# Optimization experiments

Hardware: AMD Instinct MI355X
Metric: run time of the kernel (lower is better)

Reference implementation:

```python
import jax, jax.numpy as jnp
import numpy as np

DEPTH = 16
HID = 256
INP = 256
K = 2  # arity of the complete binary tree
TOTAL = (1 << (DEPTH + 1)) - 1  # 131071 nodes, level-order indexed


def setup_inputs() -> dict:
    key = jax.random.key(0)
    ks = jax.random.split(key, 14)
    s = 1.0 / np.sqrt(HID)
    inp = {
        "x": jax.random.normal(ks[0], (TOTAL, INP), jnp.float32),
        "Wi": jax.random.normal(ks[1], (HID, INP), jnp.float32) * s,
        "bi": jax.random.normal(ks[2], (HID,), jnp.float32) * s,
        "Wf": jax.random.normal(ks[3], (HID, INP), jnp.float32) * s,
        "bf": jax.random.normal(ks[4], (HID,), jnp.float32) * s,
        "Wo": jax.random.normal(ks[5], (HID, INP), jnp.float32) * s,
        "bo": jax.random.normal(ks[6], (HID,), jnp.float32) * s,
        "Wu": jax.random.normal(ks[7], (HID, INP), jnp.float32) * s,
        "bu": jax.random.normal(ks[8], (HID,), jnp.float32) * s,
        "Ui": jax.random.normal(ks[9], (HID, HID), jnp.float32) * s,
        "Uo": jax.random.normal(ks[10], (HID, HID), jnp.float32) * s,
        "Uu": jax.random.normal(ks[11], (HID, HID), jnp.float32) * s,
        "Wfk": jax.random.normal(ks[12], (K, HID, HID), jnp.float32) * s,
        "depth": DEPTH,
    }
    return inp


def reference(x, Wi, bi, Wf, bf, Wo, bo, Wu, bu, Ui, Uo, Uu, Wfk, depth):
    sig = jax.nn.sigmoid
    H = Ui.shape[0]
    # leaf level: leaf_forward (no recurrent terms)
    start, n = (1 << depth) - 1, 1 << depth
    xs = x[start:start + n]                      # [n, INP]
    i = sig(xs @ Wi.T + bi)
    o = sig(xs @ Wo.T + bo)
    u = jnp.tanh(xs @ Wu.T + bu)
    c = i * u
    h = o * jnp.tanh(c)
    # internal levels, bottom-up
    for d in range(depth - 1, -1, -1):
        start, n = (1 << d) - 1, 1 << d
        xs = x[start:start + n]                  # [n, INP]
        hc = h.reshape(n, K, H)                  # children h (level-order)
        cc = c.reshape(n, K, H)                  # children c
        Hs = hc.sum(axis=1)                      # sum over children, [n, H]
        i = sig(xs @ Wi.T + bi + Hs @ Ui.T)
        o = sig(xs @ Wo.T + bo + Hs @ Uo.T)
        u = jnp.tanh(xs @ Wu.T + bu + Hs @ Uu.T)
        # per-child-position forget gate; original applies wf{k} to the SUM of all children h
        fx = xs @ Wf.T + bf                      # [n, H]
        ukfh = jnp.einsum('ni,koi->nko', Hs, Wfk)  # [n, K, H]
        f = sig(fx[:, None, :] + ukfh)
        c = i * u + (f * cc).sum(axis=1)
        h = o * jnp.tanh(c)
    return jnp.stack([h, c])  # [2, 1, H]: root (h, c)
```

## Files before the change

### kernel.cpp

```cpp
#include <hip/hip_runtime.h>
#include <math.h>


#define LEAF_N 65536

typedef __attribute__((ext_vector_type(8))) short bf16x8;
typedef __attribute__((ext_vector_type(4))) float f32x4;
typedef unsigned short u16;

__device__ __forceinline__ float fast_sig(float x) {
    return __builtin_amdgcn_rcpf(1.0f + __expf(-x));
}
__device__ __forceinline__ float fast_tanh(float x) {
    return 2.0f * __builtin_amdgcn_rcpf(1.0f + __expf(-2.0f * x)) - 1.0f;
}

__device__ __forceinline__ u16 f2bf(float f) {
    union { float f; unsigned u; } v; v.f = f;
    unsigned r = v.u + 0x7fffu + ((v.u >> 16) & 1u);
    return (u16)(r >> 16);
}

__host__ __device__ __forceinline__ size_t zrowOff(int d) {
    return (size_t)(65536 - (2 << d)) * 512;
}

__device__ __forceinline__ void gld_lds16(const u16* g, u16* s) {
    __builtin_amdgcn_global_load_lds(
        (const __attribute__((address_space(1))) void*)g,
        (__attribute__((address_space(3))) void*)s, 16, 0, 0);
}

template<int N> __device__ __forceinline__ void wait_vm() {
    asm volatile("s_waitcnt vmcnt(%0)" :: "n"(N) : "memory");
}

__global__ __launch_bounds__(256) void pack_weights(
    const float* __restrict__ Wi, const float* __restrict__ bi,
    const float* __restrict__ Wf, const float* __restrict__ bf,
    const float* __restrict__ Wo, const float* __restrict__ bo,
    const float* __restrict__ Wu, const float* __restrict__ bu,
    const float* __restrict__ Ui, const float* __restrict__ Uo,
    const float* __restrict__ Uu, const float* __restrict__ Wfk,
    u16* __restrict__ Wfrag, u16* __restrict__ WleafFrag,
    float* __restrict__ bbig, float* __restrict__ bleaf)
{
    int idx = blockIdx.x * 256 + threadIdx.x;
    const int NWB = 1280 * 512;
    const int NWL = 768 * 256;

    auto bigval = [&](int row, int k) -> float {
        int g = row >> 8, rr = row & 255;
        if (k < 256) {
            const float* W = (g == 0) ? Wi : (g == 1) ? Wo : (g == 2) ? Wu : Wf;
            return W[rr * 256 + k];
        }
        int kk = k - 256;
        return (g == 0) ? Ui[rr * 256 + kk]
             : (g == 1) ? Uo[rr * 256 + kk]
             : (g == 2) ? Uu[rr * 256 + kk]
             : (g == 3) ? Wfk[rr * 256 + kk]
                        : Wfk[65536 + rr * 256 + kk];
    };

    if (idx < NWB) {
        int q = idx;
        int j = q & 7, l = (q >> 3) & 63, kc = (q >> 9) & 15, nt = q >> 13;
        int row = nt * 16 + (l & 15);
        int k = kc * 32 + ((l >> 4) << 3) + j;
        Wfrag[q] = f2bf(bigval(row, k));
    } else if (idx < NWB + NWL) {
        int q = idx - NWB;
        int j = q & 7, l = (q >> 3) & 63, kc = (q >> 9) & 7, nt = q >> 12;
        int row = nt * 16 + (l & 15);
        int k = kc * 32 + ((l >> 4) << 3) + j;
        int g = row >> 8, rr = row & 255;
        const float* W = (g == 0) ? Wi : (g == 1) ? Wo : Wu;
        WleafFrag[q] = f2bf(W[rr * 256 + k]);
    } else if (idx < NWB + NWL + 1280) {
        int r = idx - NWB - NWL;
        int g = r >> 8, rr = r & 255;
        bbig[r] = (g == 0) ? bi[rr] : (g == 1) ? bo[rr] : (g == 2) ? bu[rr] : bf[rr];
    } else if (idx < NWB + NWL + 1280 + 768) {
        int r = idx - NWB - NWL - 1280;
        int g = r >> 8, rr = r & 255;
        bleaf[r] = (g == 0) ? bi[rr] : (g == 1) ? bo[rr] : bu[rr];
    }
}

__global__ __launch_bounds__(256) void cvt_all(
    const float* __restrict__ x, u16* __restrict__ Zrow,
    u16* __restrict__ Ztiles, u16* __restrict__ Xbf)
{
    int idx = blockIdx.x * 256 + threadIdx.x;
    if (idx >= 131071 * 32) return;
    int row = idx >> 5, k8 = idx & 31;
    const float* s = x + (size_t)row * 256 + k8 * 8;
    u16 r[8];
#pragma unroll
    for (int i = 0; i < 8; i++) r[i] = f2bf(s[i]);
    if (row < 65535) {
        int d = 31 - __clz(row + 1);
        int jn = row - ((1 << d) - 1);
        if (d >= 5) {
            *(uint4*)(Zrow + zrowOff(d) + (size_t)jn * 512 + k8 * 8) = *(uint4*)r;
        } else {
            int kc = k8 >> 2;
            int l = (jn & 15) + ((k8 & 3) << 4);
            size_t dst = (size_t)(4 - d) * 8192 + ((size_t)kc * 64 + l) * 8;
            *(uint4*)(Ztiles + dst) = *(uint4*)r;
        }
    } else {
        int jn = row - 65535;
        *(uint4*)(Xbf + (size_t)jn * 256 + k8 * 8) = *(uint4*)r;
    }
}

template<int KD, int NCH>
__global__ __launch_bounds__(512, 2) void gate_gemm(
    const u16* __restrict__ A, int M,
    const u16* __restrict__ Wf, const float* __restrict__ bias,
    _Float16* __restrict__ G, int chunks_per)
{
    constexpr int NSL = KD / 64;
    constexpr int KC  = KD / 32;
    constexpr int NC  = NCH * 256;
    extern __shared__ u16 As[];

    const int tid  = threadIdx.x;
    const int wave = tid >> 6;
    const int lane = tid & 63;
    const int bm = blockIdx.x * 128;
    const int nc0 = blockIdx.y * chunks_per;
    if (nc0 >= NCH) return;
    int ncEnd = nc0 + chunks_per; if (ncEnd > NCH) ncEnd = NCH;

    {
        const int srow = lane >> 3;
        const int scol = ((lane & 7) ^ srow) * 8;
#pragma unroll
        for (int kc = 0; kc < NSL; ++kc) {
#pragma unroll
            for (int q = 0; q < 2; ++q) {
                const int g = wave * 2 + q;
                gld_lds16(A + (size_t)(bm + g * 8 + srow) * KD + kc * 64 + scol,
                          As + kc * 8192 + g * 512 + lane * 8);
            }
        }
    }

    const int wr = wave >> 2;
    const int wc = wave & 3;
    const int wm = wr * 64;
    const int lm = lane & 15, q4 = lane >> 4;

    const u16* sa = As + (wm + lm) * 64;

    for (int nc = nc0; nc < ncEnd; ++nc) {
        f32x4 acc[4][4] = {};
        const u16* wfb = Wf + ((size_t)(nc * 16 + wc * 4) * KC) * 512 + lane * 8;

#pragma unroll
        for (int kc8 = 0; kc8 < NSL; ++kc8) {
            if (nc == nc0) {
#define WVM(k) case k: wait_vm<(2*(NSL-1-(k)) > 0 ? 2*(NSL-1-(k)) : 0)>(); break;
                switch (kc8) { WVM(0) WVM(1) WVM(2) WVM(3) WVM(4) WVM(5) WVM(6) WVM(7) }
#undef WVM
                __builtin_amdgcn_s_barrier();
                __builtin_amdgcn_sched_barrier(0);
            }
#pragma unroll
            for (int kk = 0; kk < 64; kk += 32) {
                const int sw = ((((kk >> 3) + q4) ^ (lm & 7)) << 3);
                const int kc = kc8 * 2 + (kk >> 5);
                bf16x8 af[4], bfr[4];
#pragma unroll
                for (int i = 0; i < 4; i++)
                    af[i] = *(const bf16x8*)(sa + kc8 * 8192 + i * 1024 + sw);
#pragma unroll
                for (int j = 0; j < 4; j++)
                    bfr[j] = *(const bf16x8*)(wfb + (size_t)(j * KC + kc) * 512);
#pragma unroll
                for (int i = 0; i < 4; i++)
#pragma unroll
                    for (int j = 0; j < 4; j++)
                        acc[i][j] = __builtin_amdgcn_mfma_f32_16x16x32_bf16(
                            af[i], bfr[j], acc[i][j], 0, 0, 0);
            }
        }

        const int cr0 = q4 * 4;
#pragma unroll
        for (int i = 0; i < 4; i++) {
#pragma unroll
            for (int j = 0; j < 4; j++) {
                const int cg = nc * 256 + wc * 64 + j * 16 + lm;
                const float bb = bias[cg];
                const bool istan = ((cg >> 8) == 2);
#pragma unroll
                for (int reg = 0; reg < 4; reg++) {
                    const int rr = bm + wm + i * 16 + cr0 + reg;
                    if (rr >= M) continue;
                    float v = acc[i][j][reg] + bb;
                    G[(size_t)rr * NC + cg] =
                        (_Float16)(istan ? fast_tanh(v) : fast_sig(v));
                }
            }
        }
    }
}

template<bool LEAF>
__global__ __launch_bounds__(256) void combine(
    const _Float16* __restrict__ G, const float* __restrict__ csrc,
    float* __restrict__ cdst, u16* __restrict__ zrow_parent,
    u16* __restrict__ zfrag_parent)
{
    constexpr int NC = LEAF ? 768 : 1280;
    const int p = blockIdx.x, h = threadIdx.x;
    const _Float16* G0 = G + (size_t)(2 * p) * NC;
    const _Float16* G1 = G0 + NC;
    float i0 = (float)G0[h], o0 = (float)G0[256 + h], u0 = (float)G0[512 + h];
    float i1 = (float)G1[h], o1 = (float)G1[256 + h], u1 = (float)G1[512 + h];
    float c0 = i0 * u0, c1 = i1 * u1;
    if (!LEAF) {
        float f00 = (float)G0[768 + h], f10 = (float)G0[1024 + h];
        float f01 = (float)G1[768 + h], f11 = (float)G1[1024 + h];
        c0 += f00 * csrc[(size_t)(4 * p) * 256 + h]
            + f10 * csrc[(size_t)(4 * p + 1) * 256 + h];
        c1 += f01 * csrc[(size_t)(4 * p + 2) * 256 + h]
            + f11 * csrc[(size_t)(4 * p + 3) * 256 + h];
    }
    float h0 = o0 * fast_tanh(c0), h1 = o1 * fast_tanh(c1);
    cdst[(size_t)(2 * p) * 256 + h] = c0;
    cdst[(size_t)(2 * p) * 256 + 256 + h] = c1;
    u16 hs = f2bf(h0 + h1);
    if (zrow_parent) {
        zrow_parent[(size_t)p * 512 + 256 + h] = hs;
    } else {
        size_t a = (((size_t)8 + (h >> 5)) * 64
                    + (p & 15) + (((h >> 3) & 3) << 4)) * 8 + (h & 7);
        zfrag_parent[a] = hs;
    }
}

__global__ __launch_bounds__(64) void small_gemm(
    const u16* __restrict__ Zpk, const u16* __restrict__ Wfrag,
    const float* __restrict__ bias, float* __restrict__ pre, int n)
{
    const int lane = threadIdx.x;
    const int q = blockIdx.x;
    const int nt0 = (q >> 2) * 16 + (q & 3) * 4;
    const int cc = lane & 15, rq = (lane >> 4) * 4;

    f32x4 acc[4] = {};
    const u16* aB = Zpk + (size_t)lane * 8;
    const u16* bB = Wfrag + ((size_t)nt0 * 16 * 64 + lane) * 8;

    bf16x8 aX, bX[4], aY, bY[4];
    aX = *(const bf16x8*)(aB);
#pragma unroll
    for (int j = 0; j < 4; ++j)
        bX[j] = *(const bf16x8*)(bB + (size_t)(j * 16) * 512);

#pragma unroll
    for (int kc = 0; kc < 16; kc += 2) {
        aY = *(const bf16x8*)(aB + (size_t)(kc + 1) * 512);
#pragma unroll
        for (int j = 0; j < 4; ++j)
            bY[j] = *(const bf16x8*)(bB + (size_t)(j * 16 + kc + 1) * 512);
#pragma unroll
        for (int j = 0; j < 4; ++j)
            acc[j] = __builtin_amdgcn_mfma_f32_16x16x32_bf16(aX, bX[j], acc[j], 0, 0, 0);
        if (kc + 2 < 16) {
            aX = *(const bf16x8*)(aB + (size_t)(kc + 2) * 512);
#pragma unroll
            for (int j = 0; j < 4; ++j)
                bX[j] = *(const bf16x8*)(bB + (size_t)(j * 16 + kc + 2) * 512);
        }
#pragma unroll
        for (int j = 0; j < 4; ++j)
            acc[j] = __builtin_amdgcn_mfma_f32_16x16x32_bf16(aY, bY[j], acc[j], 0, 0, 0);
    }

#pragma unroll
    for (int j = 0; j < 4; ++j) {
        int coln = (nt0 + j) * 16 + cc;
        float bb = bias[coln];
#pragma unroll
        for (int r = 0; r < 4; ++r) {
            int row = rq + r;
            if (row < n) pre[(size_t)row * 1280 + coln] = acc[j][r] + bb;
        }
    }
}

__global__ __launch_bounds__(256) void epi_small(
    const float* __restrict__ pre, const float* __restrict__ csrc,
    float* __restrict__ c_out, u16* __restrict__ zfrag_parent,
    float* __restrict__ root_out, int npairs)
{
    int idx = blockIdx.x * 256 + threadIdx.x;
    if (root_out) {
        int h = idx;
        const float* p = pre;
        float c = fast_sig(p[h]) * fast_tanh(p[512 + h])
                + fast_sig(p[768 + h]) * csrc[h]
                + fast_sig(p[1024 + h]) * csrc[256 + h];
        root_out[h] = fast_sig(p[256 + h]) * fast_tanh(c);
        root_out[256 + h] = c;
        return;
    }
    if (idx >= npairs * 256) return;
    int pI = idx >> 8, h = idx & 255;
    int n0 = 2 * pI;
    const float* p0 = pre + (size_t)n0 * 1280;
    const float* p1 = p0 + 1280;
    float c0 = fast_sig(p0[h]) * fast_tanh(p0[512 + h])
             + fast_sig(p0[768 + h]) * csrc[(size_t)(2 * n0) * 256 + h]
             + fast_sig(p0[1024 + h]) * csrc[(size_t)(2 * n0 + 1) * 256 + h];
    float c1 = fast_sig(p1[h]) * fast_tanh(p1[512 + h])
             + fast_sig(p1[768 + h]) * csrc[(size_t)(2 * n0 + 2) * 256 + h]
             + fast_sig(p1[1024 + h]) * csrc[(size_t)(2 * n0 + 3) * 256 + h];
    float h0 = fast_sig(p0[256 + h]) * fast_tanh(c0);
    float h1 = fast_sig(p1[256 + h]) * fast_tanh(c1);
    c_out[(size_t)n0 * 256 + h] = c0;
    c_out[(size_t)(n0 + 1) * 256 + h] = c1;
    size_t a = (((size_t)8 + (h >> 5)) * 64
                + (pI & 15) + (((h >> 3) & 3) << 4)) * 8 + (h & 7);
    zfrag_parent[a] = f2bf(h0 + h1);
}

extern "C" void kernel_launch(void* const* d_in, const int* in_sizes, int n_in,
                              void* d_out, int out_size, void* d_ws, size_t ws_size,
                              hipStream_t stream)
{
    const float* x   = (const float*)d_in[0];
    const float* Wi  = (const float*)d_in[1];
    const float* bi  = (const float*)d_in[2];
    const float* Wf  = (const float*)d_in[3];
    const float* bf  = (const float*)d_in[4];
    const float* Wo  = (const float*)d_in[5];
    const float* bo  = (const float*)d_in[6];
    const float* Wu  = (const float*)d_in[7];
    const float* bu  = (const float*)d_in[8];
    const float* Ui  = (const float*)d_in[9];
    const float* Uo  = (const float*)d_in[10];
    const float* Uu  = (const float*)d_in[11];
    const float* Wfk = (const float*)d_in[12];
    float* out = (float*)d_out;
    char* ws   = (char*)d_ws;
    (void)ws_size; (void)in_sizes; (void)n_in; (void)out_size;

    size_t off = 0;
    u16* Wfrag     = (u16*)(ws + off); off += (size_t)1280 * 512 * 2;
    u16* WleafFrag = (u16*)(ws + off); off += (size_t)768 * 256 * 2;
    float* bbig   = (float*)(ws + off); off += 1280 * 4;
    float* bleaf  = (float*)(ws + off); off += 768 * 4 + 192;
    u16* Xbf    = (u16*)(ws + off); off += (size_t)65536 * 256 * 2;
    u16* Zrow   = (u16*)(ws + off); off += (size_t)65536 * 512 * 2;
    u16* Ztiles = (u16*)(ws + off); off += (size_t)5 * 8192 * 2;
    float* cA = (float*)(ws + off); off += (size_t)65536 * 256 * 4;
    float* cB = (float*)(ws + off); off += (size_t)32768 * 256 * 4;
    float* pre_small = (float*)(ws + off); off += (size_t)16 * 1280 * 4;
    _Float16* Ghalf = (_Float16*)(ws + off); off += (size_t)65536 * 768 * 2;

    auto ztile = [&](int d) -> u16* { return Ztiles + (size_t)(4 - d) * 8192; };

    static bool attr_set = false;
    if (!attr_set) {
        hipFuncSetAttribute((const void*)gate_gemm<512, 5>,
                            hipFuncAttributeMaxDynamicSharedMemorySize, 131072);
        hipFuncSetAttribute((const void*)gate_gemm<256, 3>,
                            hipFuncAttributeMaxDynamicSharedMemorySize, 65536);
        attr_set = true;
    }

    pack_weights<<<3336, 256, 0, stream>>>(Wi, bi, Wf, bf, Wo, bo, Wu, bu,
                                           Ui, Uo, Uu, Wfk, Wfrag, WleafFrag,
                                           bbig, bleaf);
    cvt_all<<<16385, 256, 0, stream>>>(x, Zrow, Ztiles, Xbf);

    gate_gemm<256, 3><<<dim3(LEAF_N / 128, 1), 512, 65536, stream>>>(
        Xbf, LEAF_N, WleafFrag, bleaf, Ghalf, 3);
    combine<true><<<LEAF_N / 2, 256, 0, stream>>>(
        Ghalf, nullptr, cA, Zrow + zrowOff(15), nullptr);

    for (int d = 15; d >= 5; d--) {
        int n = 1 << d;
        float* csrc = (d & 1) ? cA : cB;
        float* cdst = (d & 1) ? cB : cA;
        int bx = (n + 127) / 128;
        int cs = 256 / bx; if (cs < 1) cs = 1; if (cs > 5) cs = 5;
        int cp = (5 + cs - 1) / cs;
        gate_gemm<512, 5><<<dim3(bx, cs), 512, 131072, stream>>>(
            Zrow + zrowOff(d), n, Wfrag, bbig, Ghalf, cp);
        if (d >= 6)
            combine<false><<<n / 2, 256, 0, stream>>>(
                Ghalf, csrc, cdst, Zrow + zrowOff(d - 1), nullptr);
        else
            combine<false><<<n / 2, 256, 0, stream>>>(
                Ghalf, csrc, cdst, nullptr, ztile(4));
    }

    for (int d = 4; d >= 1; d--) {
        int n = 1 << d;
        float* csrc = (d & 1) ? cA : cB;
        float* cdst = (d & 1) ? cB : cA;
        small_gemm<<<20, 64, 0, stream>>>(ztile(d), Wfrag, bbig, pre_small, n);
        epi_small<<<n / 2, 256, 0, stream>>>(pre_small, csrc, cdst,
                                             ztile(d - 1), nullptr, n / 2);
    }

    small_gemm<<<20, 64, 0, stream>>>(ztile(0), Wfrag, bbig, pre_small, 1);
    epi_small<<<1, 256, 0, stream>>>(pre_small, cB, nullptr, nullptr, out, 0);
}
```

Measured before the change: 844.2 us.

## Restructure gate GEMM into double-buffered K-tiled kernel with per-block column tiles

Replaces the gate GEMM, which loaded the whole A row-block into up to 128KB of dynamic LDS and looped over column chunks inside a block. It now uses 256-thread blocks that each own one 256-column tile from grid.y and stream A in 64-wide K slices through a static double-buffered 32KB LDS. The aim is lower LDS use for better occupancy, overlap of the next slice's load with MFMA work, and more blocks on small levels. In exchange each wave holds 8x4 accumulators (more registers), A is re-read once per column tile, and there is a barrier on every K step.

```diff
diff --git a/kernel.cpp b/kernel.cpp
--- a/kernel.cpp
+++ b/kernel.cpp
@@ -29,10 +29,6 @@
     __builtin_amdgcn_global_load_lds(
         (const __attribute__((address_space(1))) void*)g,
         (__attribute__((address_space(3))) void*)s, 16, 0, 0);
-}
-
-template<int N> __device__ __forceinline__ void wait_vm() {
-    asm volatile("s_waitcnt vmcnt(%0)" :: "n"(N) : "memory");
 }
 
 __global__ __launch_bounds__(256) void pack_weights(
@@ -116,95 +112,84 @@
     }
 }
 
-template<int KD, int NCH>
-__global__ __launch_bounds__(512, 2) void gate_gemm(
+template<int KCT, int NC>
+__global__ __launch_bounds__(256, 2) void gate_gemm(
     const u16* __restrict__ A, int M,
-    const u16* __restrict__ Wf, const float* __restrict__ bias,
-    _Float16* __restrict__ G, int chunks_per)
-{
-    constexpr int NSL = KD / 64;
-    constexpr int KC  = KD / 32;
-    constexpr int NC  = NCH * 256;
-    extern __shared__ u16 As[];
+    const u16* __restrict__ Wfrag, const float* __restrict__ bias,
+    _Float16* __restrict__ G)
+{
+    constexpr int K  = KCT * 32;
+    constexpr int NT = KCT / 2;
+    __shared__ u16 As[2][128 * 64];
 
     const int tid  = threadIdx.x;
     const int wave = tid >> 6;
     const int lane = tid & 63;
     const int bm = blockIdx.x * 128;
-    const int nc0 = blockIdx.y * chunks_per;
-    if (nc0 >= NCH) return;
-    int ncEnd = nc0 + chunks_per; if (ncEnd > NCH) ncEnd = NCH;
-
-    {
-        const int srow = lane >> 3;
-        const int scol = ((lane & 7) ^ srow) * 8;
-#pragma unroll
-        for (int kc = 0; kc < NSL; ++kc) {
-#pragma unroll
-            for (int q = 0; q < 2; ++q) {
-                const int g = wave * 2 + q;
-                gld_lds16(A + (size_t)(bm + g * 8 + srow) * KD + kc * 64 + scol,
-                          As + kc * 8192 + g * 512 + lane * 8);
+    const int bn = blockIdx.y * 256;
+
+    const int srow = lane >> 3;
+    const int scol = ((lane & 7) ^ srow) * 8;
+    const int lm = lane & 15, q4 = lane >> 4;
+
+    auto stage = [&](int bi, int t) {
+#pragma unroll
+        for (int q = 0; q < 4; ++q) {
+            const int g = wave * 4 + q;
+            gld_lds16(A + (size_t)(bm + g * 8 + srow) * K + t * 64 + scol,
+                      As[bi] + g * 512 + lane * 8);
+        }
+    };
+
+    f32x4 acc[8][4] = {};
+
+    stage(0, 0);
+    __syncthreads();
+
+#pragma unroll
+    for (int t = 0; t < NT; ++t) {
+        if (t + 1 < NT) stage((t + 1) & 1, t + 1);
+
+        const u16* Ab = As[t & 1];
+#pragma unroll
+        for (int kk = 0; kk < 64; kk += 32) {
+            const int sw = ((((kk >> 3) + q4) ^ (lm & 7)) << 3);
+            const int kc = t * 2 + (kk >> 5);
+            bf16x8 bfr[4], af[8];
+#pragma unroll
+            for (int j = 0; j < 4; j++) {
+                const int nt = (bn >> 4) + wave * 4 + j;
+                bfr[j] = *(const bf16x8*)(Wfrag +
+                              ((size_t)nt * KCT + kc) * 512 + lane * 8);
             }
-        }
-    }
-
-    const int wr = wave >> 2;
-    const int wc = wave & 3;
-    const int wm = wr * 64;
-    const int lm = lane & 15, q4 = lane >> 4;
-
-    const u16* sa = As + (wm + lm) * 64;
-
-    for (int nc = nc0; nc < ncEnd; ++nc) {
-        f32x4 acc[4][4] = {};
-        const u16* wfb = Wf + ((size_t)(nc * 16 + wc * 4) * KC) * 512 + lane * 8;
-
-#pragma unroll
-        for (int kc8 = 0; kc8 < NSL; ++kc8) {
-            if (nc == nc0) {
-#define WVM(k) case k: wait_vm<(2*(NSL-1-(k)) > 0 ? 2*(NSL-1-(k)) : 0)>(); break;
-                switch (kc8) { WVM(0) WVM(1) WVM(2) WVM(3) WVM(4) WVM(5) WVM(6) WVM(7) }
-#undef WVM
-                __builtin_amdgcn_s_barrier();
-                __builtin_amdgcn_sched_barrier(0);
-            }
-#pragma unroll
-            for (int kk = 0; kk < 64; kk += 32) {
-                const int sw = ((((kk >> 3) + q4) ^ (lm & 7)) << 3);
-                const int kc = kc8 * 2 + (kk >> 5);
-                bf16x8 af[4], bfr[4];
-#pragma unroll
-                for (int i = 0; i < 4; i++)
-                    af[i] = *(const bf16x8*)(sa + kc8 * 8192 + i * 1024 + sw);
+#pragma unroll
+            for (int i = 0; i < 8; i++)
+                af[i] = *(const bf16x8*)(Ab + (i * 16 + lm) * 64 + sw);
+#pragma unroll
+            for (int i = 0; i < 8; i++)
 #pragma unroll
                 for (int j = 0; j < 4; j++)
-                    bfr[j] = *(const bf16x8*)(wfb + (size_t)(j * KC + kc) * 512);
-#pragma unroll
-                for (int i = 0; i < 4; i++)
-#pragma unroll
-                    for (int j = 0; j < 4; j++)
-                        acc[i][j] = __builtin_amdgcn_mfma_f32_16x16x32_bf16(
-                            af[i], bfr[j], acc[i][j], 0, 0, 0);
-            }
-        }
-
-        const int cr0 = q4 * 4;
-#pragma unroll
-        for (int i = 0; i < 4; i++) {
-#pragma unroll
-            for (int j = 0; j < 4; j++) {
-                const int cg = nc * 256 + wc * 64 + j * 16 + lm;
-                const float bb = bias[cg];
-                const bool istan = ((cg >> 8) == 2);
-#pragma unroll
-                for (int reg = 0; reg < 4; reg++) {
-                    const int rr = bm + wm + i * 16 + cr0 + reg;
-                    if (rr >= M) continue;
-                    float v = acc[i][j][reg] + bb;
-                    G[(size_t)rr * NC + cg] =
-                        (_Float16)(istan ? fast_tanh(v) : fast_sig(v));
-                }
+                    acc[i][j] = __builtin_amdgcn_mfma_f32_16x16x32_bf16(
+                        af[i], bfr[j], acc[i][j], 0, 0, 0);
+        }
+        __syncthreads();
+    }
+
+    const int cr0 = q4 * 4;
+#pragma unroll
+    for (int i = 0; i < 8; i++) {
+#pragma unroll
+        for (int j = 0; j < 4; j++) {
+            const int cg = bn + wave * 64 + j * 16 + lm;
+            const float bb = bias[cg];
+            const bool istan = ((cg >> 8) == 2);
+#pragma unroll
+            for (int reg = 0; reg < 4; reg++) {
+                const int rr = bm + i * 16 + cr0 + reg;
+                if (rr >= M) continue;
+                float v = acc[i][j][reg] + bb;
+                G[(size_t)rr * NC + cg] =
+                    (_Float16)(istan ? fast_tanh(v) : fast_sig(v));
             }
         }
     }
@@ -367,22 +352,13 @@
 
     auto ztile = [&](int d) -> u16* { return Ztiles + (size_t)(4 - d) * 8192; };
 
-    static bool attr_set = false;
-    if (!attr_set) {
-        hipFuncSetAttribute((const void*)gate_gemm<512, 5>,
-                            hipFuncAttributeMaxDynamicSharedMemorySize, 131072);
-        hipFuncSetAttribute((const void*)gate_gemm<256, 3>,
-                            hipFuncAttributeMaxDynamicSharedMemorySize, 65536);
-        attr_set = true;
-    }
-
     pack_weights<<<3336, 256, 0, stream>>>(Wi, bi, Wf, bf, Wo, bo, Wu, bu,
                                            Ui, Uo, Uu, Wfk, Wfrag, WleafFrag,
                                            bbig, bleaf);
     cvt_all<<<16385, 256, 0, stream>>>(x, Zrow, Ztiles, Xbf);
 
-    gate_gemm<256, 3><<<dim3(LEAF_N / 128, 1), 512, 65536, stream>>>(
-        Xbf, LEAF_N, WleafFrag, bleaf, Ghalf, 3);
+    gate_gemm<8, 768><<<dim3(LEAF_N / 128, 3), 256, 0, stream>>>(
+        Xbf, LEAF_N, WleafFrag, bleaf, Ghalf);
     combine<true><<<LEAF_N / 2, 256, 0, stream>>>(
         Ghalf, nullptr, cA, Zrow + zrowOff(15), nullptr);
 
@@ -390,11 +366,8 @@
         int n = 1 << d;
         float* csrc = (d & 1) ? cA : cB;
         float* cdst = (d & 1) ? cB : cA;
-        int bx = (n + 127) / 128;
-        int cs = 256 / bx; if (cs < 1) cs = 1; if (cs > 5) cs = 5;
-        int cp = (5 + cs - 1) / cs;
-        gate_gemm<512, 5><<<dim3(bx, cs), 512, 131072, stream>>>(
-            Zrow + zrowOff(d), n, Wfrag, bbig, Ghalf, cp);
+        gate_gemm<16, 1280><<<dim3((n + 127) / 128, 5), 256, 0, stream>>>(
+            Zrow + zrowOff(d), n, Wfrag, bbig, Ghalf);
         if (d >= 6)
             combine<false><<<n / 2, 256, 0, stream>>>(
                 Ghalf, csrc, cdst, Zrow + zrowOff(d - 1), nullptr);
```

Result: slower. 880.9 us (+4.3%).
